# Kernel tuning notes

Hardware: AMD Instinct MI355X
Metric: run time of the kernel (lower is better)

## Reference

```python
import jax, jax.numpy as jnp
import numpy as np

T, N = 256, 4096
DL, DA, DV = 768, 74, 47
HD, NH = 8, 4  # attention hidden_dim per head, num heads
EPS = 1e-5


def setup_inputs() -> dict:
    key = jax.random.key(0)
    ks = jax.random.split(key, 40)
    rn = lambda k, s, sc=0.05: jax.random.normal(k, s, jnp.float32) * sc
    inp = {
        'l': jax.random.normal(ks[0], (N, DL), jnp.float32),
        'a': jax.random.normal(ks[1], (T, N, DA), jnp.float32),
        'v': jax.random.normal(ks[2], (T, N, DV), jnp.float32),
        # Subnet(768): 768->128->32
        'lW1': rn(ks[3], (128, DL)), 'lb1': rn(ks[4], (128,)),
        'lW2': rn(ks[5], (32, 128)), 'lb2': rn(ks[6], (32,)),
        # LSTMSubNet(74,32,32)
        'aWih': rn(ks[7], (4 * 32, DA)), 'aWhh': rn(ks[8], (4 * 32, 32)),
        'abih': rn(ks[9], (4 * 32,)), 'abhh': rn(ks[10], (4 * 32,)),
        'aWo': rn(ks[11], (32, 32)), 'abo': rn(ks[12], (32,)),
        # LSTMSubNet(47,32,32)
        'vWih': rn(ks[13], (4 * 32, DV)), 'vWhh': rn(ks[14], (4 * 32, 32)),
        'vbih': rn(ks[15], (4 * 32,)), 'vbhh': rn(ks[16], (4 * 32,)),
        'vWo': rn(ks[17], (32, 32)), 'vbo': rn(ks[18], (32,)),
        # 4 heads of SHattention (stacked): Linear(32, 8) each for Q/K/V
        'Wq': rn(ks[19], (NH, HD, 32)), 'bq': rn(ks[20], (NH, HD)),
        'Wk': rn(ks[21], (NH, HD, 32)), 'bk': rn(ks[22], (NH, HD)),
        'Wv': rn(ks[23], (NH, HD, 32)), 'bv': rn(ks[24], (NH, HD)),
        'Wz': rn(ks[25], (32, NH * HD)), 'bz': rn(ks[26], (32,)),
        'Wff': rn(ks[27], (32, 32)), 'bff': rn(ks[28], (32,)),
        'g1': jnp.ones((3, 32), jnp.float32), 'be1': jnp.zeros((3, 32), jnp.float32),
        'g2': jnp.ones((3, 32), jnp.float32), 'be2': jnp.zeros((3, 32), jnp.float32),
        # PF: 96->32->2
        'Wp1': rn(ks[29], (32, 96)), 'bp1': rn(ks[30], (32,)),
        'Wp2': rn(ks[31], (2, 32)), 'bp2': rn(ks[32], (2,)),
    }
    return inp


def _lstm_last_h(x, Wih, Whh, bih, bhh):
    # x: [T, N, D]; PyTorch LSTMCell gate order: i, f, g, o
    n, h = x.shape[1], Whh.shape[1]
    h0 = jnp.zeros((n, h), x.dtype)
    c0 = jnp.zeros((n, h), x.dtype)

    def step(carry, xt):
        hp, cp = carry
        gates = xt @ Wih.T + bih + hp @ Whh.T + bhh
        i, f, g, o = jnp.split(gates, 4, axis=-1)
        c = jax.nn.sigmoid(f) * cp + jax.nn.sigmoid(i) * jnp.tanh(g)
        hn = jax.nn.sigmoid(o) * jnp.tanh(c)
        return (hn, c), None

    (hT, _), _ = jax.lax.scan(step, (h0, c0), x)
    return hT


def _layernorm_2d(x, g, b):
    # LayerNorm over last two dims [3, 32] jointly
    mu = x.mean(axis=(1, 2), keepdims=True)
    var = ((x - mu) ** 2).mean(axis=(1, 2), keepdims=True)
    return (x - mu) * jax.lax.rsqrt(var + EPS) * g + b


def _forward(l, a, v, lW1, lb1, lW2, lb2, aWih, aWhh, abih, abhh, aWo, abo,
             vWih, vWhh, vbih, vbhh, vWo, vbo, Wq, bq, Wk, bk, Wv, bv,
             Wz, bz, Wff, bff, g1, be1, g2, be2, Wp1, bp1, Wp2, bp2):
    # modality subnets (dropout = identity in eval)
    lf = jax.nn.relu(jax.nn.relu(l @ lW1.T + lb1) @ lW2.T + lb2)          # [N, 32]
    af = jax.nn.relu(_lstm_last_h(a, aWih, aWhh, abih, abhh) @ aWo.T + abo)
    vf = jax.nn.relu(_lstm_last_h(v, vWih, vWhh, vbih, vbhh) @ vWo.T + vbo)
    x = jnp.stack([lf, af, vf], axis=1)                                   # [N, 3, 32]

    # Transformer block
    z = _layernorm_2d(x, g1, be1)
    Q = jnp.einsum('nsd,hed->nhse', z, Wq) + bq[None, :, None, :]          # [N, H, 3, 8]
    K = jnp.einsum('nsd,hed->nhse', z, Wk) + bk[None, :, None, :]
    V = jnp.einsum('nsd,hed->nhse', z, Wv) + bv[None, :, None, :]
    # NOTE: faithful to source -- softmax FIRST, then divide by sqrt(d)
    att = jax.nn.softmax(jnp.einsum('nhse,nhte->nhst', Q, K), axis=-1) / np.sqrt(HD)
    Zh = jnp.einsum('nhst,nhte->nhse', att, V)                             # [N, H, 3, 8]
    Zc = Zh.transpose(0, 2, 1, 3).reshape(Zh.shape[0], 3, NH * HD)         # concat heads
    z2 = Zc @ Wz.T + bz + x                                                # residual 1
    Zn = _layernorm_2d(z2, g2, be2)
    Z = Zn @ Wff.T + bff + z2                                              # residual 2

    # post-fusion head
    flat = Z.reshape(Z.shape[0], -1)                                       # [N, 96]
    h = jax.nn.relu(flat @ Wp1.T + bp1)
    return jax.nn.softmax(h @ Wp2.T + bp2, axis=-1)                        # [N, 2]


def reference(l, a, v, lW1, lb1, lW2, lb2, aWih, aWhh, abih, abhh, aWo, abo,
              vWih, vWhh, vbih, vbhh, vWo, vbo, Wq, bq, Wk, bk, Wv, bv,
              Wz, bz, Wff, bff, g1, be1, g2, be2, Wp1, bp1, Wp2, bp2):
    return _forward(l, a, v, lW1, lb1, lW2, lb2, aWih, aWhh, abih, abhh, aWo, abo,
                    vWih, vWhh, vbih, vbhh, vWo, vbo, Wq, bq, Wk, bk, Wv, bv,
                    Wz, bz, Wff, bff, g1, be1, g2, be2, Wp1, bp1, Wp2, bp2)
```

## Files before the change

kernel.cpp:

```cpp
#include <hip/hip_runtime.h>


typedef float float4v __attribute__((ext_vector_type(4)));
typedef float float2v __attribute__((ext_vector_type(2)));
typedef short short8v __attribute__((ext_vector_type(8)));
typedef unsigned uint2v __attribute__((ext_vector_type(2)));

#define N_SAMPLES 4096
#define T_STEPS 256
#define HSTR 40
#define HBUF (16 * HSTR)

#define LGKM0 asm volatile("s_waitcnt lgkmcnt(0)" ::: "memory")
#define VM0 asm volatile("s_waitcnt vmcnt(0)" ::: "memory")

__device__ __forceinline__ short bf16r(float f) {
  unsigned u = __float_as_uint(f);
  u += 0x7FFFu + ((u >> 16) & 1u);
  return (short)(u >> 16);
}
__device__ __forceinline__ unsigned cvt_pk_bf16(float lo, float hi) {
  unsigned r;
  asm("v_cvt_pk_bf16_f32 %0, %1, %2" : "=v"(r) : "v"(lo), "v"(hi));
  return r;
}
__device__ __forceinline__ float sigm_(float x) {
  return __builtin_amdgcn_rcpf(1.0f +
                               __builtin_amdgcn_exp2f(x * -1.44269504f));
}
__device__ __forceinline__ float tanh_(float x) {
  return 1.0f - 2.0f * __builtin_amdgcn_rcpf(
                           1.0f + __builtin_amdgcn_exp2f(x * 2.88539009f));
}
__device__ __forceinline__ float4v mfma32(short8v a, short8v b, float4v c) {
  return __builtin_amdgcn_mfma_f32_16x16x32_bf16(a, b, c, 0, 0, 0);
}
__device__ __forceinline__ void gld16(const float* g, float* l) {
  __builtin_amdgcn_global_load_lds(
      (const __attribute__((address_space(1))) unsigned int*)g,
      (__attribute__((address_space(3))) unsigned int*)l, 16, 0, 0);
}

#define SMEM_BYTES 28736

template <int D, int NK32>
__device__ void lstm2w(const float* __restrict__ x,
                       const float* __restrict__ Wih,
                       const float* __restrict__ Whh,
                       const float* __restrict__ bih,
                       const float* __restrict__ bhh,
                       const float* __restrict__ Wo,
                       const float* __restrict__ bo,
                       float* __restrict__ outf, int n0, char* smem) {
  constexpr int FPS = 16 * D;
  constexpr int UPS = FPS / 4;
  constexpr int FULL = UPS / 64;
  constexpr int REM = UPS % 64;

  float* xbuf = (float*)smem;
  unsigned short* Hu = (unsigned short*)(smem + 4 * FPS * 4 + 64);

  const int tid = threadIdx.x;
  const int wid = tid >> 6;
  const int lane = tid & 63;
  const int c = lane & 15;
  const int q = lane >> 4;

  auto stageslot = [&](int t) {
    const float* gs = x + (size_t)t * (N_SAMPLES * D) + (size_t)n0 * D;
    float* ls = xbuf + (t & 3) * FPS;
#pragma unroll
    for (int r = 0; r < FULL; ++r)
      gld16(gs + (r * 64 + lane) * 4, ls + r * 256);
    if (REM) {
      if (lane < REM) gld16(gs + (FULL * 64 + lane) * 4, ls + FULL * 256);
    }
  };

  if (wid == 0) { stageslot(0); stageslot(2); }
  else          { stageslot(1); }

  short8v wfx[4][NK32], wfh[4];
  float4v binit[4];
#pragma unroll
  for (int T = 0; T < 4; ++T) {
    const int G = (c & 3) * 32 + wid * 16 + (c >> 2) * 4 + T;
    const float* wr = Wih + G * D;
#pragma unroll
    for (int kt = 0; kt < NK32; ++kt) {
      short8v s;
#pragma unroll
      for (int e = 0; e < 8; ++e) {
        const int d = kt * 32 + q * 8 + e;
        s[e] = (d < D) ? bf16r(wr[d]) : (short)0;
      }
      wfx[T][kt] = s;
    }
    const float* hr = Whh + G * 32;
#pragma unroll
    for (int e = 0; e < 8; ++e) wfh[T][e] = bf16r(hr[q * 8 + e]);
#pragma unroll
    for (int r = 0; r < 4; ++r) {
      const int Gr = r * 32 + wid * 16 + q * 4 + T;
      binit[T][r] = bih[Gr] + bhh[Gr];
    }
  }

  {
    unsigned* Hz = (unsigned*)Hu;
    for (int i = tid; i < 640; i += 128) Hz[i] = 0;
  }

  VM0;
  LGKM0;
  __builtin_amdgcn_s_barrier();

  auto ldcvt = [&](const float* xs0, short8v* xo) {
    const float* xs = xs0 + c * D;
#pragma unroll
    for (int kt = 0; kt < NK32; ++kt) {
      const float* p = xs + kt * 32 + q * 8;
      const float2v r0 = *(const float2v*)(p);
      const float2v r1 = *(const float2v*)(p + 2);
      const float2v r2 = *(const float2v*)(p + 4);
      const float2v r3 = *(const float2v*)(p + 6);
      union { short8v s; unsigned u[4]; } fr;
      fr.u[0] = cvt_pk_bf16(r0[0], r0[1]);
      fr.u[1] = cvt_pk_bf16(r1[0], r1[1]);
      fr.u[2] = cvt_pk_bf16(r2[0], r2[1]);
      fr.u[3] = cvt_pk_bf16(r3[0], r3[1]);
      xo[kt] = fr.s;
    }
  };

  float cst[4] = {0.0f, 0.0f, 0.0f, 0.0f};
  float4v gxA[4], gxB[4];
  {
    short8v xF[NK32];
    ldcvt(xbuf, xF);
#pragma unroll
    for (int T = 0; T < 4; ++T) {
      float4v g4 = binit[T];
#pragma unroll
      for (int kt = 0; kt < NK32; ++kt) g4 = mfma32(wfx[T][kt], xF[kt], g4);
      gxA[T] = g4;
    }
  }

  auto STEP = [&](int t, int i, float4v (&gc)[4], float4v (&gn)[4]) {
    const int pb = i & 1;
    const short8v hB = *(const short8v*)(Hu + pb * HBUF + c * HSTR + q * 8);
    if (((i + 3) & 1) == wid && t + 3 < T_STEPS) stageslot(t + 3);
    short8v xN[NK32];
    ldcvt(xbuf + ((i + 1) & 3) * FPS, xN);
#pragma unroll
    for (int T = 0; T < 4; ++T) {
      float4v g4 = binit[T];
#pragma unroll
      for (int kt = 0; kt < NK32; ++kt) g4 = mfma32(wfx[T][kt], xN[kt], g4);
      gn[T] = g4;
    }
    __builtin_amdgcn_s_setprio(1);
    float hv[4];
#pragma unroll
    for (int T = 0; T < 4; ++T) {
      const float4v acc = mfma32(wfh[T], hB, gc[T]);
      const float iv = sigm_(acc[0]);
      const float fv = sigm_(acc[1]);
      const float gv = tanh_(acc[2]);
      const float ov = sigm_(acc[3]);
      const float cv = fv * cst[T] + iv * gv;
      cst[T] = cv;
      hv[T] = ov * tanh_(cv);
    }
    uint2v hp;
    hp[0] = cvt_pk_bf16(hv[0], hv[1]);
    hp[1] = cvt_pk_bf16(hv[2], hv[3]);
    *(uint2v*)(Hu + (1 - pb) * HBUF + c * HSTR + wid * 16 + q * 4) = hp;
    __builtin_amdgcn_s_setprio(0);
    LGKM0;
    if ((i & 1) == wid) { VM0; }
    __builtin_amdgcn_s_barrier();
  };

  for (int tb = 0; tb < T_STEPS; tb += 8) {
    STEP(tb + 0, 0, gxA, gxB);
    STEP(tb + 1, 1, gxB, gxA);
    STEP(tb + 2, 2, gxA, gxB);
    STEP(tb + 3, 3, gxB, gxA);
    STEP(tb + 4, 0, gxA, gxB);
    STEP(tb + 5, 1, gxB, gxA);
    STEP(tb + 6, 2, gxA, gxB);
    STEP(tb + 7, 3, gxB, gxA);
  }

  {
    const short8v hB = *(const short8v*)(Hu + c * HSTR + q * 8);
    const float* wor = Wo + (16 * wid + c) * 32;
    short8v w8;
#pragma unroll
    for (int e = 0; e < 8; ++e) w8[e] = bf16r(wor[q * 8 + e]);
    float4v o4 = {0.0f, 0.0f, 0.0f, 0.0f};
    o4 = mfma32(w8, hB, o4);
    float4v res;
#pragma unroll
    for (int r = 0; r < 4; ++r)
      res[r] = fmaxf(o4[r] + bo[16 * wid + q * 4 + r], 0.0f);
    *(float4v*)(outf + (size_t)(n0 + c) * 32 + 16 * wid + q * 4) = res;
  }
}

__device__ void lf8(const float* __restrict__ l, const float* __restrict__ lW1,
                    const float* __restrict__ lb1,
                    const float* __restrict__ lW2,
                    const float* __restrict__ lb2, float* __restrict__ lf,
                    int n0, char* smem) {
  float* lsh = (float*)smem;
  float* h1sh = lsh + 8 * 768;
  const int tid = threadIdx.x;

  {
    const float4v* src = (const float4v*)(l + (size_t)n0 * 768);
    float4v* dst = (float4v*)lsh;
#pragma unroll
    for (int i = 0; i < 12; ++i) dst[tid + i * 128] = src[tid + i * 128];
  }
  __syncthreads();

  {
    const int u = tid;
    float acc[8];
#pragma unroll
    for (int i = 0; i < 8; ++i) acc[i] = 0.0f;
    const float4v* wrow = (const float4v*)(lW1 + u * 768);
    for (int k4 = 0; k4 < 192; ++k4) {
      const float4v w = wrow[k4];
#pragma unroll
      for (int i = 0; i < 8; ++i) {
        const float4v xv = ((const float4v*)(lsh + i * 768))[k4];
        acc[i] += w[0] * xv[0] + w[1] * xv[1] + w[2] * xv[2] + w[3] * xv[3];
      }
    }
    const float b = lb1[u];
#pragma unroll
    for (int i = 0; i < 8; ++i)
      h1sh[i * 128 + u] = fmaxf(acc[i] + b, 0.0f);
  }
  __syncthreads();

  {
    const int u2 = tid & 31;
    const int sg = tid >> 5;
    float acc0 = 0.0f, acc1 = 0.0f;
    const float4v* w2 = (const float4v*)(lW2 + u2 * 128);
#pragma unroll
    for (int k4 = 0; k4 < 32; ++k4) {
      const float4v w = w2[k4];
      const float4v xa = ((const float4v*)(h1sh + sg * 128))[k4];
      const float4v xb = ((const float4v*)(h1sh + (sg + 4) * 128))[k4];
      acc0 += w[0] * xa[0] + w[1] * xa[1] + w[2] * xa[2] + w[3] * xa[3];
      acc1 += w[0] * xb[0] + w[1] * xb[1] + w[2] * xb[2] + w[3] * xb[3];
    }
    const float b2 = lb2[u2];
    lf[(size_t)(n0 + sg) * 32 + u2] = fmaxf(acc0 + b2, 0.0f);
    lf[(size_t)(n0 + sg + 4) * 32 + u2] = fmaxf(acc1 + b2, 0.0f);
  }
}

__global__ __launch_bounds__(128, 2) void front_kernel(
    const float* __restrict__ a, const float* __restrict__ v,
    const float* __restrict__ aWih, const float* __restrict__ aWhh,
    const float* __restrict__ abih, const float* __restrict__ abhh,
    const float* __restrict__ aWo, const float* __restrict__ abo,
    const float* __restrict__ vWih, const float* __restrict__ vWhh,
    const float* __restrict__ vbih, const float* __restrict__ vbhh,
    const float* __restrict__ vWo, const float* __restrict__ vbo,
    const float* __restrict__ l, const float* __restrict__ lW1,
    const float* __restrict__ lb1, const float* __restrict__ lW2,
    const float* __restrict__ lb2, float* __restrict__ lfw,
    float* __restrict__ afw, float* __restrict__ vfw) {
  __shared__ __align__(16) char smem[SMEM_BYTES];
  const int b = blockIdx.x;
  if (b < 512) {
    lf8(l, lW1, lb1, lW2, lb2, lfw, b * 8, smem);
  } else if (b < 768) {
    lstm2w<74, 3>(a, aWih, aWhh, abih, abhh, aWo, abo, afw, (b - 512) * 16,
                  smem);
  } else {
    lstm2w<47, 2>(v, vWih, vWhh, vbih, vbhh, vWo, vbo, vfw, (b - 768) * 16,
                  smem);
  }
}

__global__ __launch_bounds__(256) void head_kernel(
    const float* __restrict__ lf, const float* __restrict__ af,
    const float* __restrict__ vf, const float* __restrict__ Wq,
    const float* __restrict__ bq, const float* __restrict__ Wk,
    const float* __restrict__ bk, const float* __restrict__ Wv,
    const float* __restrict__ bv, const float* __restrict__ Wz,
    const float* __restrict__ bz, const float* __restrict__ Wff,
    const float* __restrict__ bff, const float* __restrict__ g1,
    const float* __restrict__ be1, const float* __restrict__ g2,
    const float* __restrict__ be2, const float* __restrict__ Wp1,
    const float* __restrict__ bp1, const float* __restrict__ Wp2,
    const float* __restrict__ bp2, float* __restrict__ out) {
  __shared__ float shA[8][3][33];
  __shared__ float shB[8][3][33];
  const int tid = threadIdx.x;
  const int j = tid & 31;
  const int slot = tid >> 5;
  const int n = blockIdx.x * 8 + slot;
  const size_t off = (size_t)n * 32 + j;

  const float x0 = lf[off], x1 = af[off], x2 = vf[off];

  auto ln3 = [&](float a0, float a1, float a2, const float* g,
                 const float* be, float* o) {
    float s = a0 + a1 + a2;
    s += __shfl_xor(s, 1); s += __shfl_xor(s, 2); s += __shfl_xor(s, 4);
    s += __shfl_xor(s, 8); s += __shfl_xor(s, 16);
    const float mu = s * (1.0f / 96.0f);
    const float d0 = a0 - mu, d1 = a1 - mu, d2 = a2 - mu;
    float ss = d0 * d0 + d1 * d1 + d2 * d2;
    ss += __shfl_xor(ss, 1); ss += __shfl_xor(ss, 2); ss += __shfl_xor(ss, 4);
    ss += __shfl_xor(ss, 8); ss += __shfl_xor(ss, 16);
    const float rs = rsqrtf(ss * (1.0f / 96.0f) + 1e-5f);
    o[0] = d0 * rs * g[j] + be[j];
    o[1] = d1 * rs * g[32 + j] + be[32 + j];
    o[2] = d2 * rs * g[64 + j] + be[64 + j];
  };

  float z[3];
  ln3(x0, x1, x2, g1, be1, z);
  shA[slot][0][j] = z[0]; shA[slot][1][j] = z[1]; shA[slot][2][j] = z[2];
  __syncthreads();

  float qv[3], kv[3], vv[3];
  {
    const float bqj = bq[j], bkj = bk[j], bvj = bv[j];
    qv[0] = bqj; qv[1] = bqj; qv[2] = bqj;
    kv[0] = bkj; kv[1] = bkj; kv[2] = bkj;
    vv[0] = bvj; vv[1] = bvj; vv[2] = bvj;
    const float* wqr = Wq + j * 32;
    const float* wkr = Wk + j * 32;
    const float* wvr = Wv + j * 32;
#pragma unroll 8
    for (int k = 0; k < 32; ++k) {
      const float zz0 = shA[slot][0][k], zz1 = shA[slot][1][k],
                  zz2 = shA[slot][2][k];
      const float wq = wqr[k], wk_ = wkr[k], wv_ = wvr[k];
      qv[0] += wq * zz0;  qv[1] += wq * zz1;  qv[2] += wq * zz2;
      kv[0] += wk_ * zz0; kv[1] += wk_ * zz1; kv[2] += wk_ * zz2;
      vv[0] += wv_ * zz0; vv[1] += wv_ * zz1; vv[2] += wv_ * zz2;
    }
  }

  float at[3][3];
#pragma unroll
  for (int s = 0; s < 3; ++s)
#pragma unroll
    for (int t2 = 0; t2 < 3; ++t2) {
      float p = qv[s] * kv[t2];
      p += __shfl_xor(p, 1); p += __shfl_xor(p, 2); p += __shfl_xor(p, 4);
      at[s][t2] = p;
    }
#pragma unroll
  for (int s = 0; s < 3; ++s) {
    const float m = fmaxf(fmaxf(at[s][0], at[s][1]), at[s][2]);
    const float e0 = __expf(at[s][0] - m), e1 = __expf(at[s][1] - m),
                e2 = __expf(at[s][2] - m);
    const float sc = 0.35355339059327373f * __fdividef(1.0f, e0 + e1 + e2);
    at[s][0] = e0 * sc; at[s][1] = e1 * sc; at[s][2] = e2 * sc;
  }
  float zc[3];
#pragma unroll
  for (int s = 0; s < 3; ++s)
    zc[s] = at[s][0] * vv[0] + at[s][1] * vv[1] + at[s][2] * vv[2];
  shB[slot][0][j] = zc[0]; shB[slot][1][j] = zc[1]; shB[slot][2][j] = zc[2];
  __syncthreads();

  const float bzj = bz[j];
  float z2a[3] = {bzj + x0, bzj + x1, bzj + x2};
  {
    const float* wzr = Wz + j * 32;
#pragma unroll 8
    for (int k = 0; k < 32; ++k) {
      const float w = wzr[k];
      z2a[0] += w * shB[slot][0][k];
      z2a[1] += w * shB[slot][1][k];
      z2a[2] += w * shB[slot][2][k];
    }
  }

  float zn[3];
  ln3(z2a[0], z2a[1], z2a[2], g2, be2, zn);
  shA[slot][0][j] = zn[0]; shA[slot][1][j] = zn[1]; shA[slot][2][j] = zn[2];
  __syncthreads();

  const float bffj = bff[j];
  float Za[3] = {bffj + z2a[0], bffj + z2a[1], bffj + z2a[2]};
  {
    const float* wfr = Wff + j * 32;
#pragma unroll 8
    for (int k = 0; k < 32; ++k) {
      const float w = wfr[k];
      Za[0] += w * shA[slot][0][k];
      Za[1] += w * shA[slot][1][k];
      Za[2] += w * shA[slot][2][k];
    }
  }
  shB[slot][0][j] = Za[0]; shB[slot][1][j] = Za[1]; shB[slot][2][j] = Za[2];
  __syncthreads();

  float p = bp1[j];
  {
    const float* wpr = Wp1 + j * 96;
#pragma unroll
    for (int s = 0; s < 3; ++s)
#pragma unroll 8
      for (int k = 0; k < 32; ++k) p += wpr[s * 32 + k] * shB[slot][s][k];
  }
  p = fmaxf(p, 0.0f);
  float l0 = Wp2[j] * p, l1 = Wp2[32 + j] * p;
  l0 += __shfl_xor(l0, 1); l0 += __shfl_xor(l0, 2); l0 += __shfl_xor(l0, 4);
  l0 += __shfl_xor(l0, 8); l0 += __shfl_xor(l0, 16);
  l1 += __shfl_xor(l1, 1); l1 += __shfl_xor(l1, 2); l1 += __shfl_xor(l1, 4);
  l1 += __shfl_xor(l1, 8); l1 += __shfl_xor(l1, 16);
  l0 += bp2[0]; l1 += bp2[1];
  const float mx = fmaxf(l0, l1);
  const float e0 = __expf(l0 - mx), e1 = __expf(l1 - mx);
  const float inv = __fdividef(1.0f, e0 + e1);
  if (j == 0) {
    out[(size_t)n * 2 + 0] = e0 * inv;
    out[(size_t)n * 2 + 1] = e1 * inv;
  }
}

extern "C" void kernel_launch(void* const* d_in, const int* in_sizes, int n_in,
                              void* d_out, int out_size, void* d_ws,
                              size_t ws_size, hipStream_t stream) {
  const float* l    = (const float*)d_in[0];
  const float* a    = (const float*)d_in[1];
  const float* v    = (const float*)d_in[2];
  const float* lW1  = (const float*)d_in[3];
  const float* lb1  = (const float*)d_in[4];
  const float* lW2  = (const float*)d_in[5];
  const float* lb2  = (const float*)d_in[6];
  const float* aWih = (const float*)d_in[7];
  const float* aWhh = (const float*)d_in[8];
  const float* abih = (const float*)d_in[9];
  const float* abhh = (const float*)d_in[10];
  const float* aWo  = (const float*)d_in[11];
  const float* abo  = (const float*)d_in[12];
  const float* vWih = (const float*)d_in[13];
  const float* vWhh = (const float*)d_in[14];
  const float* vbih = (const float*)d_in[15];
  const float* vbhh = (const float*)d_in[16];
  const float* vWo  = (const float*)d_in[17];
  const float* vbo  = (const float*)d_in[18];
  const float* Wq   = (const float*)d_in[19];
  const float* bq   = (const float*)d_in[20];
  const float* Wk   = (const float*)d_in[21];
  const float* bk   = (const float*)d_in[22];
  const float* Wv   = (const float*)d_in[23];
  const float* bv   = (const float*)d_in[24];
  const float* Wz   = (const float*)d_in[25];
  const float* bz   = (const float*)d_in[26];
  const float* Wff  = (const float*)d_in[27];
  const float* bff  = (const float*)d_in[28];
  const float* g1   = (const float*)d_in[29];
  const float* be1  = (const float*)d_in[30];
  const float* g2   = (const float*)d_in[31];
  const float* be2  = (const float*)d_in[32];
  const float* Wp1  = (const float*)d_in[33];
  const float* bp1  = (const float*)d_in[34];
  const float* Wp2  = (const float*)d_in[35];
  const float* bp2  = (const float*)d_in[36];

  float* out = (float*)d_out;
  float* ws = (float*)d_ws;
  float* lfw = ws;
  float* afw = ws + 4096 * 32;
  float* vfw = ws + 2 * 4096 * 32;

  hipLaunchKernelGGL(front_kernel, dim3(1024), dim3(128), 0, stream, a, v,
                     aWih, aWhh, abih, abhh, aWo, abo, vWih, vWhh, vbih,
                     vbhh, vWo, vbo, l, lW1, lb1, lW2, lb2, lfw, afw, vfw);
  hipLaunchKernelGGL(head_kernel, dim3(512), dim3(256), 0, stream, lfw, afw,
                     vfw, Wq, bq, Wk, bk, Wv, bv, Wz, bz, Wff, bff, g1, be1,
                     g2, be2, Wp1, bp1, Wp2, bp2, out);
}
```

Before: 277.3 us.

## Prefetch next-step x from LDS into registers one step ahead in LSTM loop

The LDS reads of the x tile for step t+2 are issued during step t and held in registers (nxr), so the next step only converts and feeds the MFMAs without waiting on LDS latency. The global-to-LDS staging pointer now advances incrementally instead of being recomputed from t. This adds register pressure (extra float2 arrays per kt) and relies on the existing barrier and VM0 waits to keep the staged slot valid before it is read.

```diff
diff --git a/kernel.cpp b/kernel.cpp
--- a/kernel.cpp
+++ b/kernel.cpp
@@ -66,19 +66,20 @@
   const int c = lane & 15;
   const int q = lane >> 4;
 
-  auto stageslot = [&](int t) {
-    const float* gs = x + (size_t)t * (N_SAMPLES * D) + (size_t)n0 * D;
-    float* ls = xbuf + (t & 3) * FPS;
+  const float* gsrun = x + (size_t)wid * (N_SAMPLES * D) + (size_t)n0 * D;
+
+  auto stageslot = [&](float* ls) {
 #pragma unroll
     for (int r = 0; r < FULL; ++r)
-      gld16(gs + (r * 64 + lane) * 4, ls + r * 256);
+      gld16(gsrun + (r * 64 + lane) * 4, ls + r * 256);
     if (REM) {
-      if (lane < REM) gld16(gs + (FULL * 64 + lane) * 4, ls + FULL * 256);
-    }
+      if (lane < REM) gld16(gsrun + (FULL * 64 + lane) * 4, ls + FULL * 256);
+    }
+    gsrun += 2 * (N_SAMPLES * D);
   };
 
-  if (wid == 0) { stageslot(0); stageslot(2); }
-  else          { stageslot(1); }
+  if (wid == 0) { stageslot(xbuf); stageslot(xbuf + 2 * FPS); }
+  else          { stageslot(xbuf + 1 * FPS); }
 
   short8v wfx[4][NK32], wfh[4];
   float4v binit[4];
@@ -115,8 +116,13 @@
   LGKM0;
   __builtin_amdgcn_s_barrier();
 
-  auto ldcvt = [&](const float* xs0, short8v* xo) {
-    const float* xs = xs0 + c * D;
+  float cst[4] = {0.0f, 0.0f, 0.0f, 0.0f};
+  float4v gxA[4], gxB[4];
+  float2v nxr[NK32][4];
+
+  {
+    const float* xs = xbuf + c * D;
+    short8v xF[NK32];
 #pragma unroll
     for (int kt = 0; kt < NK32; ++kt) {
       const float* p = xs + kt * 32 + q * 8;
@@ -129,15 +135,8 @@
       fr.u[1] = cvt_pk_bf16(r1[0], r1[1]);
       fr.u[2] = cvt_pk_bf16(r2[0], r2[1]);
       fr.u[3] = cvt_pk_bf16(r3[0], r3[1]);
-      xo[kt] = fr.s;
-    }
-  };
-
-  float cst[4] = {0.0f, 0.0f, 0.0f, 0.0f};
-  float4v gxA[4], gxB[4];
-  {
-    short8v xF[NK32];
-    ldcvt(xbuf, xF);
+      xF[kt] = fr.s;
+    }
 #pragma unroll
     for (int T = 0; T < 4; ++T) {
       float4v g4 = binit[T];
@@ -145,20 +144,49 @@
       for (int kt = 0; kt < NK32; ++kt) g4 = mfma32(wfx[T][kt], xF[kt], g4);
       gxA[T] = g4;
     }
+    const float* xs1 = xbuf + FPS + c * D;
+#pragma unroll
+    for (int kt = 0; kt < NK32; ++kt) {
+      const float* p = xs1 + kt * 32 + q * 8;
+      nxr[kt][0] = *(const float2v*)(p);
+      nxr[kt][1] = *(const float2v*)(p + 2);
+      nxr[kt][2] = *(const float2v*)(p + 4);
+      nxr[kt][3] = *(const float2v*)(p + 6);
+    }
   }
 
   auto STEP = [&](int t, int i, float4v (&gc)[4], float4v (&gn)[4]) {
     const int pb = i & 1;
+    const bool mystage = (((i + 3) & 1) == wid);
     const short8v hB = *(const short8v*)(Hu + pb * HBUF + c * HSTR + q * 8);
-    if (((i + 3) & 1) == wid && t + 3 < T_STEPS) stageslot(t + 3);
+    if (mystage && t + 3 < T_STEPS) stageslot(xbuf + ((i + 3) & 3) * FPS);
     short8v xN[NK32];
-    ldcvt(xbuf + ((i + 1) & 3) * FPS, xN);
+#pragma unroll
+    for (int kt = 0; kt < NK32; ++kt) {
+      union { short8v s; unsigned u[4]; } fr;
+      fr.u[0] = cvt_pk_bf16(nxr[kt][0][0], nxr[kt][0][1]);
+      fr.u[1] = cvt_pk_bf16(nxr[kt][1][0], nxr[kt][1][1]);
+      fr.u[2] = cvt_pk_bf16(nxr[kt][2][0], nxr[kt][2][1]);
+      fr.u[3] = cvt_pk_bf16(nxr[kt][3][0], nxr[kt][3][1]);
+      xN[kt] = fr.s;
+    }
 #pragma unroll
     for (int T = 0; T < 4; ++T) {
       float4v g4 = binit[T];
 #pragma unroll
       for (int kt = 0; kt < NK32; ++kt) g4 = mfma32(wfx[T][kt], xN[kt], g4);
       gn[T] = g4;
+    }
+    {
+      const float* xs2 = xbuf + ((i + 2) & 3) * FPS + c * D;
+#pragma unroll
+      for (int kt = 0; kt < NK32; ++kt) {
+        const float* p = xs2 + kt * 32 + q * 8;
+        nxr[kt][0] = *(const float2v*)(p);
+        nxr[kt][1] = *(const float2v*)(p + 2);
+        nxr[kt][2] = *(const float2v*)(p + 4);
+        nxr[kt][3] = *(const float2v*)(p + 6);
+      }
     }
     __builtin_amdgcn_s_setprio(1);
     float hv[4];
@@ -179,7 +207,7 @@
     *(uint2v*)(Hu + (1 - pb) * HBUF + c * HSTR + wid * 16 + q * 4) = hp;
     __builtin_amdgcn_s_setprio(0);
     LGKM0;
-    if ((i & 1) == wid) { VM0; }
+    if (mystage) { VM0; }
     __builtin_amdgcn_s_barrier();
   };
 
```

Measured after the change: 231.9 us. 16.4% less time.
